# Kernel tuning notes

Measured on AMD Instinct MI355X. Metric: run time of the kernel, lower is better.

## Reference

```python
import jax, jax.numpy as jnp
import numpy as np

B, D, O = 16384, 1024, 1024
NUM_TASKS = 2
E = 4  # experts per group (2 task groups + 1 shared group)


def setup_inputs() -> dict:
    key = jax.random.key(0)
    ks = jax.random.split(key, 7)
    x = jax.random.normal(ks[0], (B, D), dtype=jnp.float32)
    # Stacked expert params: groups g in {task0, task1, shared}, each with E experts.
    W = jax.random.normal(ks[1], (3, E, D, O), dtype=jnp.float32) * 0.02  # Linear weight (in,out layout)
    b = jax.random.normal(ks[2], (3, E, O), dtype=jnp.float32) * 0.02
    # Per-task gates over (E specific + E shared) = 8 experts.
    Wg = jax.random.normal(ks[3], (NUM_TASKS, D, 2 * E), dtype=jnp.float32) * 0.02
    bg = jax.random.normal(ks[4], (NUM_TASKS, 2 * E), dtype=jnp.float32) * 0.02
    # Shared gate over all 3*E = 12 experts (is_top=False).
    Wgs = jax.random.normal(ks[5], (D, 3 * E), dtype=jnp.float32) * 0.02
    bgs = jax.random.normal(ks[6], (3 * E,), dtype=jnp.float32) * 0.02
    return {"x": x, "W": W, "b": b, "Wg": Wg, "bg": bg, "Wgs": Wgs, "bgs": bgs}


def reference(x, W, b, Wg, bg, Wgs, bgs):
    # All 12 experts share the same input (single-input branch): one batched GEMM.
    # h: [3, B, E, O]  (dropout is identity in eval mode)
    h = jax.nn.relu(jnp.einsum('bd,gedo->gbeo', x, W) + b[:, None, :, :])
    # Per-task gates: [T, B, 2E]
    sel_t = jax.nn.softmax(jnp.einsum('bd,tdm->tbm', x, Wg) + bg[:, None, :], axis=-1)
    outs = []
    for t in range(NUM_TASKS):
        mat = jnp.concatenate([h[t], h[2]], axis=1)  # [B, 2E, O]
        outs.append(jnp.einsum('bmo,bm->bo', mat, sel_t[t]))
    # Shared gate over all experts (is_top=False): [B, 3E]
    sel_s = jax.nn.softmax(x @ Wgs + bgs, axis=-1)
    mat_all = jnp.concatenate([h[0], h[1], h[2]], axis=1)  # [B, 3E, O]
    outs.append(jnp.einsum('bmo,bm->bo', mat_all, sel_s))
    return tuple(outs)
```

## Files before the change

kernel.cpp:

```cpp
#include <hip/hip_runtime.h>

typedef unsigned short ushort_t;
typedef __attribute__((ext_vector_type(8))) short short8;
typedef __attribute__((ext_vector_type(4))) float floatx4;

#define B_ROWS 16384
#define BO 16777216
#define MC 4096

__device__ __forceinline__ ushort_t f2bf(float f){
  unsigned u = __float_as_uint(f);
  u += 0x7fffu + ((u >> 16) & 1u);
  return (ushort_t)(u >> 16);
}
__device__ __forceinline__ float bf2f(ushort_t u){
  return __uint_as_float(((unsigned)u) << 16);
}

__device__ __forceinline__ void gld_lds16(void* l, const void* g){
  __builtin_amdgcn_global_load_lds(
      (__attribute__((address_space(1))) void*)(g),
      (__attribute__((address_space(3))) void*)(l), 16, 0, 0);
}

__global__ void cvt_x(const float* __restrict__ x, ushort_t* __restrict__ xb){
  const int i = (blockIdx.x * 256 + threadIdx.x) * 4;
  const floatx4 v = *(const floatx4*)(x + i);
  ushort4 o;
  o.x = f2bf(v[0]); o.y = f2bf(v[1]); o.z = f2bf(v[2]); o.w = f2bf(v[3]);
  *(ushort4*)(xb + i) = o;
}

__global__ void cvt_wt(const float* __restrict__ W, ushort_t* __restrict__ wt){
  __shared__ float t[64][65];
  const int blk = blockIdx.x;
  const int ge = blk >> 8, dt = (blk >> 4) & 15, ot = blk & 15;
  const float* src = W + ((size_t)ge << 20) + (size_t)(dt * 64) * 1024 + ot * 64;
  const int c4 = (threadIdx.x & 15) * 4, r0 = threadIdx.x >> 4;
#pragma unroll
  for (int p = 0; p < 4; ++p){
    const int r = r0 + p * 16;
    const floatx4 v = *(const floatx4*)(src + (size_t)r * 1024 + c4);
    t[r][c4] = v[0]; t[r][c4+1] = v[1]; t[r][c4+2] = v[2]; t[r][c4+3] = v[3];
  }
  __syncthreads();
  ushort_t* dst = wt + ((size_t)ge << 20) + (size_t)(ot * 64) * 1024 + dt * 64;
  const int d4 = (threadIdx.x & 15) * 4, o0 = threadIdx.x >> 4;
#pragma unroll
  for (int p = 0; p < 4; ++p){
    const int o = o0 + p * 16;
    ushort4 ov;
    ov.x = f2bf(t[d4][o]);   ov.y = f2bf(t[d4+1][o]);
    ov.z = f2bf(t[d4+2][o]); ov.w = f2bf(t[d4+3][o]);
    *(ushort4*)(dst + (size_t)o * 1024 + d4) = ov;
  }
}

__global__ void cvt_wg(const float* __restrict__ Wg, const float* __restrict__ bg,
                       const float* __restrict__ Wgs, const float* __restrict__ bgs,
                       ushort_t* __restrict__ wgcat, float* __restrict__ biascat){
  const int m = blockIdx.x;
#pragma unroll
  for (int j = 0; j < 4; ++j){
    const int d = j * 256 + threadIdx.x;
    float v;
    if (m < 16)      v = Wg[((size_t)((m >> 3) * 1024 + d)) * 8 + (m & 7)];
    else if (m < 28) v = Wgs[(size_t)d * 12 + (m - 16)];
    else             v = 0.f;
    wgcat[m * 1024 + d] = f2bf(v);
  }
  if (threadIdx.x == 0){
    float bv;
    if (m < 16)      bv = bg[m];
    else if (m < 28) bv = bgs[m - 16];
    else             bv = -1e30f;
    biascat[m] = bv;
  }
}

__global__ __launch_bounds__(256) void gates_mfma(
    const ushort_t* __restrict__ xb, const ushort_t* __restrict__ wgcat,
    const float* __restrict__ biascat, float* __restrict__ selT)
{
  __shared__ __align__(16) char gsm[20480];
  const int tid = threadIdx.x;
  const int lane = tid & 63;
  const int w = tid >> 6;
  const int lr = lane & 15;
  const int brow = blockIdx.x * 128;

  const int sc = (((tid & 7) ^ ((tid >> 3) & 7)) << 4);
  const char* aS = (const char*)xb + (size_t)(brow + (tid >> 3)) * 2048 + sc;
  const char* bS = (const char*)wgcat + (size_t)(tid >> 3) * 2048 + sc;

  const int kx0 = (((lane >> 4) << 4)) ^ ((lane & 7) << 4);
  const int kx1 = (64 + ((lane >> 4) << 4)) ^ ((lane & 7) << 4);

  int aOff[2], bOff[2];
#pragma unroll
  for (int m = 0; m < 2; ++m) aOff[m] = (w * 32 + m * 16 + lr) * 128;
#pragma unroll
  for (int n = 0; n < 2; ++n) bOff[n] = 16384 + (n * 16 + lr) * 128;

  const floatx4 fz = {0.f, 0.f, 0.f, 0.f};
  floatx4 hacc[2][2];
#pragma unroll
  for (int m = 0; m < 2; ++m)
#pragma unroll
    for (int n = 0; n < 2; ++n) hacc[m][n] = fz;

  for (int kt = 0; kt < 16; ++kt){
    const size_t ko = (size_t)kt * 128;
#pragma unroll
    for (int j = 0; j < 4; ++j)
      gld_lds16(gsm + j * 4096 + w * 1024, aS + (size_t)j * 65536 + ko);
    gld_lds16(gsm + 16384 + w * 1024, bS + ko);
    __syncthreads();
    short8 av[2][2], bv[2][2];
#pragma unroll
    for (int m = 0; m < 2; ++m){
      av[m][0] = *(const short8*)(gsm + aOff[m] + kx0);
      av[m][1] = *(const short8*)(gsm + aOff[m] + kx1);
    }
#pragma unroll
    for (int n = 0; n < 2; ++n){
      bv[n][0] = *(const short8*)(gsm + bOff[n] + kx0);
      bv[n][1] = *(const short8*)(gsm + bOff[n] + kx1);
    }
#pragma unroll
    for (int m = 0; m < 2; ++m)
#pragma unroll
      for (int n = 0; n < 2; ++n){
        hacc[m][n] = __builtin_amdgcn_mfma_f32_16x16x32_bf16(av[m][0], bv[n][0], hacc[m][n], 0, 0, 0);
        hacc[m][n] = __builtin_amdgcn_mfma_f32_16x16x32_bf16(av[m][1], bv[n][1], hacc[m][n], 0, 0, 0);
      }
    __syncthreads();
  }

  const float bc0 = biascat[lr];
  const float bc1 = biascat[16 + lr];
#pragma unroll
  for (int m = 0; m < 2; ++m){
#pragma unroll
    for (int r = 0; r < 4; ++r){
      float l0 = hacc[m][0][r] + bc0;
      float l1 = hacc[m][1][r] + bc1;
      float mx0 = l0;
#pragma unroll
      for (int s = 1; s < 8; s <<= 1) mx0 = fmaxf(mx0, __shfl_xor(mx0, s, 64));
      float e0 = __expf(l0 - mx0);
      float s0 = e0;
#pragma unroll
      for (int s = 1; s < 8; s <<= 1) s0 += __shfl_xor(s0, s, 64);
      float mx1 = l1;
#pragma unroll
      for (int s = 1; s < 16; s <<= 1) mx1 = fmaxf(mx1, __shfl_xor(mx1, s, 64));
      float e1 = __expf(l1 - mx1);
      float s1 = e1;
#pragma unroll
      for (int s = 1; s < 16; s <<= 1) s1 += __shfl_xor(s1, s, 64);
      const int row = brow + w * 32 + m * 16 + ((lane >> 4) << 2) + r;
      selT[(size_t)lr * B_ROWS + row] = e0 / s0;
      if (lr < 12) selT[(size_t)(16 + lr) * B_ROWS + row] = e1 / s1;
    }
  }
}

__global__ __launch_bounds__(512, 2) void pass1_gemm(
    const ushort_t* __restrict__ xb,
    const ushort_t* __restrict__ wt,
    const float* __restrict__ bias,
    ushort_t* __restrict__ h,
    int chunk_row0)
{
  __shared__ __align__(16) char smem[131072];
  const int tid  = threadIdx.x;
  const int lane = tid & 63;
  const int wv   = tid >> 6;
  const int wm   = wv >> 2;
  const int wn   = wv & 3;
  const int lr   = lane & 15;

  const int bid = blockIdx.x;
  const int L = (bid & 7) * 96 + (bid >> 3);
  const int mt = L / 48;
  const int rr = L % 48;
  const int ex = rr >> 2;
  const int nt = rr & 3;
  const int brow_l = mt * 256;
  const int browg  = chunk_row0 + brow_l;
  const int bcol   = nt * 256;

  const int sc = (((tid & 7) ^ ((tid >> 3) & 7)) << 4);
  const char* aSrc[2];
  const char* bSrc[2];
#pragma unroll
  for (int hh = 0; hh < 2; ++hh){
    aSrc[hh] = (const char*)xb + (size_t)(browg + hh * 128 + (tid >> 3)) * 2048 + sc;
    bSrc[hh] = (const char*)wt + ((size_t)ex << 21)
             + (size_t)(bcol + hh * 128 + (tid >> 3)) * 2048 + sc;
  }

  auto stageA = [&](int hh, int kt, int bo){
    char* d = smem + bo + hh * 16384 + wv * 1024;
    const char* s = aSrc[hh] + (size_t)kt * 128;
    gld_lds16(d, s);
    gld_lds16(d + 8192, s + 131072);
  };
  auto stageB = [&](int hh, int kt, int bo){
    char* d = smem + bo + 32768 + hh * 16384 + wv * 1024;
    const char* s = bSrc[hh] + (size_t)kt * 128;
    gld_lds16(d, s);
    gld_lds16(d + 8192, s + 131072);
  };

  const int kx0 = (((lane >> 4) << 4)) ^ ((lane & 7) << 4);
  const int kx1 = (64 + ((lane >> 4) << 4)) ^ ((lane & 7) << 4);
  int aOff[8], bOff[4];
#pragma unroll
  for (int m = 0; m < 8; ++m) aOff[m] = wm * 16384 + (m * 16 + lr) * 128;
#pragma unroll
  for (int n = 0; n < 4; ++n)
    bOff[n] = 32768 + (wn >> 1) * 16384 + ((wn & 1) * 64 + n * 16 + lr) * 128;

  const floatx4 fz = {0.f, 0.f, 0.f, 0.f};
  floatx4 hacc[8][4];
#pragma unroll
  for (int m = 0; m < 8; ++m)
#pragma unroll
    for (int n = 0; n < 4; ++n) hacc[m][n] = fz;

  stageA(0, 0, 0); stageA(1, 0, 0); stageB(0, 0, 0); stageB(1, 0, 0);
  stageB(0, 1, 65536); stageA(0, 1, 65536); stageA(1, 1, 65536);
  asm volatile("s_waitcnt vmcnt(6)" ::: "memory");
  __builtin_amdgcn_s_barrier();

#define LDF(X) (*(const short8*)(smem + (X)))
#define MFMA_(A, Bv, C) __builtin_amdgcn_mfma_f32_16x16x32_bf16(A, Bv, C, 0, 0, 0)
#define LGKM0_SB() { asm volatile("s_waitcnt lgkmcnt(0)" ::: "memory"); __builtin_amdgcn_sched_barrier(0); }

  for (int i = 0; i < 16; ++i){
    const int cur = (i & 1) << 16;
    const int nxt = cur ^ 65536;

    short8 a0[4][2], b0[2][2];
#pragma unroll
    for (int m = 0; m < 4; ++m){
      a0[m][0] = LDF(cur + aOff[m] + kx0);
      a0[m][1] = LDF(cur + aOff[m] + kx1);
    }
#pragma unroll
    for (int n = 0; n < 2; ++n){
      b0[n][0] = LDF(cur + bOff[n] + kx0);
      b0[n][1] = LDF(cur + bOff[n] + kx1);
    }
    if (i + 1 < 16) stageB(1, i + 1, nxt);
    __builtin_amdgcn_s_barrier();
    LGKM0_SB();
    __builtin_amdgcn_s_setprio(1);
#pragma unroll
    for (int m = 0; m < 4; ++m)
#pragma unroll
      for (int n = 0; n < 2; ++n){
        hacc[m][n] = MFMA_(a0[m][0], b0[n][0], hacc[m][n]);
        hacc[m][n] = MFMA_(a0[m][1], b0[n][1], hacc[m][n]);
      }
    __builtin_amdgcn_s_setprio(0);
    __builtin_amdgcn_s_barrier();

    short8 b1[2][2];
#pragma unroll
    for (int n = 0; n < 2; ++n){
      b1[n][0] = LDF(cur + bOff[2 + n] + kx0);
      b1[n][1] = LDF(cur + bOff[2 + n] + kx1);
    }
    __builtin_amdgcn_s_barrier();
    LGKM0_SB();
    __builtin_amdgcn_s_setprio(1);
#pragma unroll
    for (int m = 0; m < 4; ++m)
#pragma unroll
      for (int n = 0; n < 2; ++n){
        hacc[m][2 + n] = MFMA_(a0[m][0], b1[n][0], hacc[m][2 + n]);
        hacc[m][2 + n] = MFMA_(a0[m][1], b1[n][1], hacc[m][2 + n]);
      }
    __builtin_amdgcn_s_setprio(0);
    __builtin_amdgcn_s_barrier();

    short8 a1[4][2];
#pragma unroll
    for (int m = 0; m < 4; ++m){
      a1[m][0] = LDF(cur + aOff[4 + m] + kx0);
      a1[m][1] = LDF(cur + aOff[4 + m] + kx1);
    }
    if (i + 2 < 16) stageB(0, i + 2, cur);
    __builtin_amdgcn_s_barrier();
    LGKM0_SB();
    __builtin_amdgcn_s_setprio(1);
#pragma unroll
    for (int m = 0; m < 4; ++m)
#pragma unroll
      for (int n = 0; n < 2; ++n){
        hacc[4 + m][n] = MFMA_(a1[m][0], b0[n][0], hacc[4 + m][n]);
        hacc[4 + m][n] = MFMA_(a1[m][1], b0[n][1], hacc[4 + m][n]);
      }
    __builtin_amdgcn_s_setprio(0);
    __builtin_amdgcn_s_barrier();

    if (i + 2 < 16) { stageA(0, i + 2, cur); stageA(1, i + 2, cur); }
    __builtin_amdgcn_s_barrier();
    __builtin_amdgcn_s_setprio(1);
#pragma unroll
    for (int m = 0; m < 4; ++m)
#pragma unroll
      for (int n = 0; n < 2; ++n){
        hacc[4 + m][2 + n] = MFMA_(a1[m][0], b1[n][0], hacc[4 + m][2 + n]);
        hacc[4 + m][2 + n] = MFMA_(a1[m][1], b1[n][1], hacc[4 + m][2 + n]);
      }
    __builtin_amdgcn_s_setprio(0);
    if (i < 14)       { asm volatile("s_waitcnt vmcnt(6)" ::: "memory"); }
    else if (i == 14) { asm volatile("s_waitcnt vmcnt(0)" ::: "memory"); }
    __builtin_amdgcn_s_barrier();
  }

  const int colb = bcol + wn * 64 + lr;
  float bi[4];
#pragma unroll
  for (int n = 0; n < 4; ++n) bi[n] = bias[ex * 1024 + colb + n * 16];
  ushort_t* hbase = h + ((size_t)ex * MC) * 1024;
#pragma unroll
  for (int m = 0; m < 8; ++m){
#pragma unroll
    for (int r = 0; r < 4; ++r){
      const int row = brow_l + wm * 128 + m * 16 + ((lane >> 4) << 2) + r;
      ushort_t* hp = hbase + (size_t)row * 1024 + colb;
#pragma unroll
      for (int n = 0; n < 4; ++n){
        float v = hacc[m][n][r] + bi[n];
        hp[n * 16] = f2bf(fmaxf(v, 0.f));
      }
    }
  }
#undef LDF
#undef MFMA_
#undef LGKM0_SB
}

__global__ __launch_bounds__(256) void combine_kernel(
    const ushort_t* __restrict__ h,
    const float* __restrict__ selT,
    float* __restrict__ out,
    int row0)
{
  const int tid = threadIdx.x;
  const int lb  = blockIdx.x * 2 + (tid >> 7);
  const int b   = row0 + lb;
  const int c   = (tid & 127) * 8;
  const ushort_t* hp = h + (size_t)lb * 1024 + c;

  float a0[8], a1[8], as_[8];
#pragma unroll
  for (int k = 0; k < 8; ++k){ a0[k] = 0.f; a1[k] = 0.f; as_[k] = 0.f; }

#pragma unroll
  for (int e = 0; e < 4; ++e){
    const float w0 = selT[(size_t)e * B_ROWS + b];
    const float ws = selT[(size_t)(16 + e) * B_ROWS + b];
    const short8 hv = *(const short8*)(hp + (size_t)e * (MC * 1024));
#pragma unroll
    for (int k = 0; k < 8; ++k){
      const float f = bf2f((ushort_t)hv[k]);
      a0[k] += w0 * f; as_[k] += ws * f;
    }
  }
#pragma unroll
  for (int e = 0; e < 4; ++e){
    const float w1 = selT[(size_t)(8 + e) * B_ROWS + b];
    const float ws = selT[(size_t)(20 + e) * B_ROWS + b];
    const short8 hv = *(const short8*)(hp + (size_t)(4 + e) * (MC * 1024));
#pragma unroll
    for (int k = 0; k < 8; ++k){
      const float f = bf2f((ushort_t)hv[k]);
      a1[k] += w1 * f; as_[k] += ws * f;
    }
  }
#pragma unroll
  for (int e = 0; e < 4; ++e){
    const float w0 = selT[(size_t)(4 + e) * B_ROWS + b];
    const float w1 = selT[(size_t)(12 + e) * B_ROWS + b];
    const float ws = selT[(size_t)(24 + e) * B_ROWS + b];
    const short8 hv = *(const short8*)(hp + (size_t)(8 + e) * (MC * 1024));
#pragma unroll
    for (int k = 0; k < 8; ++k){
      const float f = bf2f((ushort_t)hv[k]);
      a0[k] += w0 * f; a1[k] += w1 * f; as_[k] += ws * f;
    }
  }

  float* o0 = out + (size_t)b * 1024 + c;
  *(floatx4*)(o0)     = *(const floatx4*)(a0);
  *(floatx4*)(o0 + 4) = *(const floatx4*)(a0 + 4);
  float* o1 = o0 + BO;
  *(floatx4*)(o1)     = *(const floatx4*)(a1);
  *(floatx4*)(o1 + 4) = *(const floatx4*)(a1 + 4);
  float* o2 = o1 + BO;
  *(floatx4*)(o2)     = *(const floatx4*)(as_);
  *(floatx4*)(o2 + 4) = *(const floatx4*)(as_ + 4);
}

__global__ void gates_kernel(const float* __restrict__ x,
                             const float* __restrict__ Wg,
                             const float* __restrict__ bg,
                             const float* __restrict__ Wgs,
                             const float* __restrict__ bgs,
                             float* __restrict__ selT)
{
  const int lane = threadIdx.x & 63;
  const int w    = threadIdx.x >> 6;
  const int b    = blockIdx.x * 4 + w;
  const float* xr = x + (size_t)b * 1024;
  float acc[28];
#pragma unroll
  for (int m = 0; m < 28; ++m) acc[m] = 0.f;
#pragma unroll
  for (int j = 0; j < 4; ++j){
    const int d0 = (j * 64 + lane) * 4;
    const floatx4 xv = *(const floatx4*)(xr + d0);
#pragma unroll
    for (int q = 0; q < 4; ++q){
      const float xs = xv[q];
      const int d = d0 + q;
      const float* g0 = Wg + d * 8;
      const float* g1 = Wg + 8192 + d * 8;
      const float* gs = Wgs + d * 12;
#pragma unroll
      for (int m = 0; m < 8; ++m)  acc[m]      += xs * g0[m];
#pragma unroll
      for (int m = 0; m < 8; ++m)  acc[8 + m]  += xs * g1[m];
#pragma unroll
      for (int m = 0; m < 12; ++m) acc[16 + m] += xs * gs[m];
    }
  }
#pragma unroll
  for (int m = 0; m < 28; ++m){
    float v = acc[m];
#pragma unroll
    for (int off = 1; off < 64; off <<= 1) v += __shfl_xor(v, off, 64);
    acc[m] = v;
  }
  if (lane == 0){
    float e0[8], e1[8], es[12];
    float mx0 = -1e30f, mx1 = -1e30f, mxs = -1e30f;
#pragma unroll
    for (int m = 0; m < 8; ++m){  e0[m] = acc[m]      + bg[m];     mx0 = fmaxf(mx0, e0[m]); }
#pragma unroll
    for (int m = 0; m < 8; ++m){  e1[m] = acc[8 + m]  + bg[8 + m]; mx1 = fmaxf(mx1, e1[m]); }
#pragma unroll
    for (int m = 0; m < 12; ++m){ es[m] = acc[16 + m] + bgs[m];    mxs = fmaxf(mxs, es[m]); }
    float s0 = 0.f, s1 = 0.f, ss = 0.f;
#pragma unroll
    for (int m = 0; m < 8; ++m){  e0[m] = __expf(e0[m] - mx0); s0 += e0[m]; }
#pragma unroll
    for (int m = 0; m < 8; ++m){  e1[m] = __expf(e1[m] - mx1); s1 += e1[m]; }
#pragma unroll
    for (int m = 0; m < 12; ++m){ es[m] = __expf(es[m] - mxs); ss += es[m]; }
    const float r0 = 1.f / s0, r1 = 1.f / s1, rs = 1.f / ss;
#pragma unroll
    for (int m = 0; m < 8; ++m)  selT[(size_t)m * B_ROWS + b]        = e0[m] * r0;
#pragma unroll
    for (int m = 0; m < 8; ++m)  selT[(size_t)(8 + m) * B_ROWS + b]  = e1[m] * r1;
#pragma unroll
    for (int m = 0; m < 12; ++m) selT[(size_t)(16 + m) * B_ROWS + b] = es[m] * rs;
  }
}

__global__ __launch_bounds__(256, 2) void moe_kernel(
    const ushort_t* __restrict__ xb,
    const ushort_t* __restrict__ wt,
    const float* __restrict__ bias,
    const float* __restrict__ selT,
    float* __restrict__ out)
{
  __shared__ __align__(16) char smem[24576];
  const int tid  = threadIdx.x;
  const int lane = tid & 63;
  const int wid  = tid >> 6;
  const int wm   = wid >> 1;
  const int wn   = wid & 1;
  const int brow = (blockIdx.x >> 4) << 7;
  const int bcol = (blockIdx.x & 15) << 6;
  const int rstg = tid >> 3;
  const int scol = ((tid & 7) << 4) ^ ((rstg & 7) << 4);
  size_t aoff[4], boff[2];
#pragma unroll
  for (int i = 0; i < 4; ++i) aoff[i] = (size_t)(brow + i * 32 + rstg) * 2048 + scol;
#pragma unroll
  for (int i = 0; i < 2; ++i) boff[i] = (size_t)(bcol + i * 32 + rstg) * 2048 + scol;
  char* aldst = smem + wid * 1024;
  char* bldst = smem + 16384 + wid * 1024;
  const int kl   = (lane >> 4) << 4;
  const int swzr = (lane & 7) << 4;
  int arow[4], brw[2];
#pragma unroll
  for (int m = 0; m < 4; ++m) arow[m] = (wm * 64 + m * 16 + (lane & 15)) * 128;
#pragma unroll
  for (int n = 0; n < 2; ++n) brw[n] = 16384 + (wn * 32 + n * 16 + (lane & 15)) * 128;
  const floatx4 fz = {0.f, 0.f, 0.f, 0.f};
  floatx4 o0a[4][2], o1a[4][2], osa[4][2];
#pragma unroll
  for (int m = 0; m < 4; ++m)
#pragma unroll
    for (int n = 0; n < 2; ++n){ o0a[m][n] = fz; o1a[m][n] = fz; osa[m][n] = fz; }
  const int c0 = bcol + wn * 32 + (lane & 15);
  const int rb = brow + wm * 64 + ((lane >> 4) << 2);
  for (int ex = 0; ex < 12; ++ex){
    floatx4 hacc[4][2];
#pragma unroll
    for (int m = 0; m < 4; ++m)
#pragma unroll
      for (int n = 0; n < 2; ++n) hacc[m][n] = fz;
    const size_t wbase = (size_t)ex << 21;
    for (int kt = 0; kt < 16; ++kt){
      const size_t ko = (size_t)kt << 7;
#pragma unroll
      for (int i = 0; i < 4; ++i)
        gld_lds16(aldst + i * 4096, (const char*)xb + aoff[i] + ko);
#pragma unroll
      for (int i = 0; i < 2; ++i)
        gld_lds16(bldst + i * 4096, (const char*)wt + wbase + boff[i] + ko);
      __syncthreads();
#pragma unroll
      for (int kk = 0; kk < 2; ++kk){
        short8 av[4], bv[2];
        const int kb = (kk << 6) + kl;
#pragma unroll
        for (int m = 0; m < 4; ++m)
          av[m] = *(const short8*)(smem + arow[m] + (kb ^ swzr));
#pragma unroll
        for (int n = 0; n < 2; ++n)
          bv[n] = *(const short8*)(smem + brw[n] + (kb ^ swzr));
#pragma unroll
        for (int m = 0; m < 4; ++m)
#pragma unroll
          for (int n = 0; n < 2; ++n)
            hacc[m][n] = __builtin_amdgcn_mfma_f32_16x16x32_bf16(av[m], bv[n], hacc[m][n], 0, 0, 0);
      }
      __syncthreads();
    }
    const int g = ex >> 2, e = ex & 3;
    const float bi0 = bias[ex * 1024 + c0];
    const float bi1 = bias[ex * 1024 + c0 + 16];
    int i0, i1, is_;
    if (g == 0)      { i0 = e;     i1 = -1;     is_ = 16 + e; }
    else if (g == 1) { i0 = -1;    i1 = 8 + e;  is_ = 20 + e; }
    else             { i0 = 4 + e; i1 = 12 + e; is_ = 24 + e; }
#pragma unroll
    for (int m = 0; m < 4; ++m){
      const int rg = rb + m * 16;
      const floatx4 wsv = *(const floatx4*)(selT + (size_t)is_ * B_ROWS + rg);
      floatx4 w0 = fz, w1 = fz;
      if (i0 >= 0) w0 = *(const floatx4*)(selT + (size_t)i0 * B_ROWS + rg);
      if (i1 >= 0) w1 = *(const floatx4*)(selT + (size_t)i1 * B_ROWS + rg);
#pragma unroll
      for (int n = 0; n < 2; ++n){
        const float bi = n ? bi1 : bi0;
#pragma unroll
        for (int r = 0; r < 4; ++r){
          float hv = hacc[m][n][r] + bi;
          hv = fmaxf(hv, 0.f);
          osa[m][n][r] += wsv[r] * hv;
          o0a[m][n][r] += w0[r] * hv;
          o1a[m][n][r] += w1[r] * hv;
        }
      }
    }
  }
#pragma unroll
  for (int m = 0; m < 4; ++m){
#pragma unroll
    for (int n = 0; n < 2; ++n){
#pragma unroll
      for (int r = 0; r < 4; ++r){
        const size_t idx = (size_t)(rb + m * 16 + r) * 1024 + (c0 + (n << 4));
        out[idx]          = o0a[m][n][r];
        out[idx + BO]     = o1a[m][n][r];
        out[idx + 2 * BO] = osa[m][n][r];
      }
    }
  }
}

extern "C" void kernel_launch(void* const* d_in, const int* in_sizes, int n_in,
                              void* d_out, int out_size, void* d_ws, size_t ws_size,
                              hipStream_t stream) {
  const float* x   = (const float*)d_in[0];
  const float* W   = (const float*)d_in[1];
  const float* b   = (const float*)d_in[2];
  const float* Wg  = (const float*)d_in[3];
  const float* bg  = (const float*)d_in[4];
  const float* Wgs = (const float*)d_in[5];
  const float* bgs = (const float*)d_in[6];
  float* out = (float*)d_out;

  char* ws = (char*)d_ws;
  ushort_t* xb   = (ushort_t*)ws;
  ushort_t* wtp  = (ushort_t*)(ws + 33554432);
  float*    selT = (float*)(ws + 58720256);
  ushort_t* wgc  = (ushort_t*)(ws + 60555264);
  float*    bcat = (float*)(ws + 60620800);
  ushort_t* hbuf = (ushort_t*)(ws + 67108864);

  const bool two_pass = ws_size >= (size_t)(67108864 + 12 * MC * 1024 * 2);

  cvt_x<<<dim3(16384), dim3(256), 0, stream>>>(x, xb);
  cvt_wt<<<dim3(3072), dim3(256), 0, stream>>>(W, wtp);

  if (two_pass){
    cvt_wg<<<dim3(32), dim3(256), 0, stream>>>(Wg, bg, Wgs, bgs, wgc, bcat);
    gates_mfma<<<dim3(128), dim3(256), 0, stream>>>(xb, wgc, bcat, selT);
    for (int c = 0; c < 16384 / MC; ++c){
      pass1_gemm<<<dim3((MC / 256) * 48), dim3(512), 0, stream>>>(xb, wtp, b, hbuf, c * MC);
      combine_kernel<<<dim3(MC / 2), dim3(256), 0, stream>>>(hbuf, selT, out, c * MC);
    }
  } else {
    gates_kernel<<<dim3(4096), dim3(256), 0, stream>>>(x, Wg, bg, Wgs, bgs, selT);
    moe_kernel<<<dim3(2048), dim3(256), 0, stream>>>(xb, wtp, b, selT, out);
  }
}
```

Before: 606.8 us.

## Make each GEMM block loop over three experts with a persistent grid of 256

The GEMM grid drops from 768 blocks to 256. Each block now runs a 48-step K loop that covers three consecutive experts for the same 256x256 output tile, writing the bias+ReLU epilogue and resetting accumulators after every 16 steps. The aim is to keep the pipeline primed across experts, removing per-block prologue and drain and the partial last wave (768 blocks at 2 per CU over 256 CUs). The trade-off is fewer, longer blocks, epilogue stores that stall the pipeline mid-loop, and reduced reuse of the A tile in cache, since x is reloaded for each expert.

```diff
diff --git a/kernel.cpp b/kernel.cpp
--- a/kernel.cpp
+++ b/kernel.cpp
@@ -180,36 +180,37 @@
   const int wm   = wv >> 2;
   const int wn   = wv & 3;
   const int lr   = lane & 15;
+  const int NT   = 48;
 
   const int bid = blockIdx.x;
-  const int L = (bid & 7) * 96 + (bid >> 3);
-  const int mt = L / 48;
-  const int rr = L % 48;
-  const int ex = rr >> 2;
-  const int nt = rr & 3;
+  const int L = (bid & 7) * 32 + (bid >> 3);
+  const int eg = L >> 6;
+  const int nt = (L >> 4) & 3;
+  const int mt = L & 15;
   const int brow_l = mt * 256;
   const int browg  = chunk_row0 + brow_l;
   const int bcol   = nt * 256;
 
   const int sc = (((tid & 7) ^ ((tid >> 3) & 7)) << 4);
   const char* aSrc[2];
-  const char* bSrc[2];
+  size_t bOffBase[2];
 #pragma unroll
   for (int hh = 0; hh < 2; ++hh){
     aSrc[hh] = (const char*)xb + (size_t)(browg + hh * 128 + (tid >> 3)) * 2048 + sc;
-    bSrc[hh] = (const char*)wt + ((size_t)ex << 21)
-             + (size_t)(bcol + hh * 128 + (tid >> 3)) * 2048 + sc;
+    bOffBase[hh] = (size_t)(bcol + hh * 128 + (tid >> 3)) * 2048 + sc;
   }
 
   auto stageA = [&](int hh, int kt, int bo){
     char* d = smem + bo + hh * 16384 + wv * 1024;
-    const char* s = aSrc[hh] + (size_t)kt * 128;
+    const char* s = aSrc[hh] + (size_t)(kt & 15) * 128;
     gld_lds16(d, s);
     gld_lds16(d + 8192, s + 131072);
   };
   auto stageB = [&](int hh, int kt, int bo){
+    const int exk = eg * 3 + (kt >> 4);
     char* d = smem + bo + 32768 + hh * 16384 + wv * 1024;
-    const char* s = bSrc[hh] + (size_t)kt * 128;
+    const char* s = (const char*)wt + ((size_t)exk << 21) + bOffBase[hh]
+                  + (size_t)(kt & 15) * 128;
     gld_lds16(d, s);
     gld_lds16(d + 8192, s + 131072);
   };
@@ -229,6 +230,32 @@
   for (int m = 0; m < 8; ++m)
 #pragma unroll
     for (int n = 0; n < 4; ++n) hacc[m][n] = fz;
+
+  const int colb = bcol + wn * 64 + lr;
+  float bi[3][4];
+#pragma unroll
+  for (int ee = 0; ee < 3; ++ee)
+#pragma unroll
+    for (int n = 0; n < 4; ++n)
+      bi[ee][n] = bias[(eg * 3 + ee) * 1024 + colb + n * 16];
+
+  auto EPI = [&](int el){
+    ushort_t* hbase = h + ((size_t)(eg * 3 + el) * MC) * 1024;
+#pragma unroll
+    for (int m = 0; m < 8; ++m){
+#pragma unroll
+      for (int r = 0; r < 4; ++r){
+        const int row = brow_l + wm * 128 + m * 16 + ((lane >> 4) << 2) + r;
+        ushort_t* hp = hbase + (size_t)row * 1024 + colb;
+#pragma unroll
+        for (int n = 0; n < 4; ++n){
+          float v = hacc[m][n][r] + bi[el][n];
+          hp[n * 16] = f2bf(fmaxf(v, 0.f));
+          hacc[m][n][r] = 0.f;
+        }
+      }
+    }
+  };
 
   stageA(0, 0, 0); stageA(1, 0, 0); stageB(0, 0, 0); stageB(1, 0, 0);
   stageB(0, 1, 65536); stageA(0, 1, 65536); stageA(1, 1, 65536);
@@ -239,7 +266,7 @@
 #define MFMA_(A, Bv, C) __builtin_amdgcn_mfma_f32_16x16x32_bf16(A, Bv, C, 0, 0, 0)
 #define LGKM0_SB() { asm volatile("s_waitcnt lgkmcnt(0)" ::: "memory"); __builtin_amdgcn_sched_barrier(0); }
 
-  for (int i = 0; i < 16; ++i){
+  for (int i = 0; i < NT; ++i){
     const int cur = (i & 1) << 16;
     const int nxt = cur ^ 65536;
 
@@ -254,7 +281,7 @@
       b0[n][0] = LDF(cur + bOff[n] + kx0);
       b0[n][1] = LDF(cur + bOff[n] + kx1);
     }
-    if (i + 1 < 16) stageB(1, i + 1, nxt);
+    if (i + 1 < NT) stageB(1, i + 1, nxt);
     __builtin_amdgcn_s_barrier();
     LGKM0_SB();
     __builtin_amdgcn_s_setprio(1);
@@ -293,7 +320,7 @@
       a1[m][0] = LDF(cur + aOff[4 + m] + kx0);
       a1[m][1] = LDF(cur + aOff[4 + m] + kx1);
     }
-    if (i + 2 < 16) stageB(0, i + 2, cur);
+    if (i + 2 < NT) stageB(0, i + 2, cur);
     __builtin_amdgcn_s_barrier();
     LGKM0_SB();
     __builtin_amdgcn_s_setprio(1);
@@ -307,7 +334,7 @@
     __builtin_amdgcn_s_setprio(0);
     __builtin_amdgcn_s_barrier();
 
-    if (i + 2 < 16) { stageA(0, i + 2, cur); stageA(1, i + 2, cur); }
+    if (i + 2 < NT) { stageA(0, i + 2, cur); stageA(1, i + 2, cur); }
     __builtin_amdgcn_s_barrier();
     __builtin_amdgcn_s_setprio(1);
 #pragma unroll
@@ -318,28 +345,10 @@
         hacc[4 + m][2 + n] = MFMA_(a1[m][1], b1[n][1], hacc[4 + m][2 + n]);
       }
     __builtin_amdgcn_s_setprio(0);
-    if (i < 14)       { asm volatile("s_waitcnt vmcnt(6)" ::: "memory"); }
-    else if (i == 14) { asm volatile("s_waitcnt vmcnt(0)" ::: "memory"); }
-    __builtin_amdgcn_s_barrier();
-  }
-
-  const int colb = bcol + wn * 64 + lr;
-  float bi[4];
-#pragma unroll
-  for (int n = 0; n < 4; ++n) bi[n] = bias[ex * 1024 + colb + n * 16];
-  ushort_t* hbase = h + ((size_t)ex * MC) * 1024;
-#pragma unroll
-  for (int m = 0; m < 8; ++m){
-#pragma unroll
-    for (int r = 0; r < 4; ++r){
-      const int row = brow_l + wm * 128 + m * 16 + ((lane >> 4) << 2) + r;
-      ushort_t* hp = hbase + (size_t)row * 1024 + colb;
-#pragma unroll
-      for (int n = 0; n < 4; ++n){
-        float v = hacc[m][n][r] + bi[n];
-        hp[n * 16] = f2bf(fmaxf(v, 0.f));
-      }
-    }
+    if ((i & 15) == 15) EPI(i >> 4);
+    if (i < NT - 2)       { asm volatile("s_waitcnt vmcnt(6)" ::: "memory"); }
+    else if (i == NT - 2) { asm volatile("s_waitcnt vmcnt(0)" ::: "memory"); }
+    __builtin_amdgcn_s_barrier();
   }
 #undef LDF
 #undef MFMA_
@@ -619,7 +628,7 @@
     cvt_wg<<<dim3(32), dim3(256), 0, stream>>>(Wg, bg, Wgs, bgs, wgc, bcat);
     gates_mfma<<<dim3(128), dim3(256), 0, stream>>>(xb, wgc, bcat, selT);
     for (int c = 0; c < 16384 / MC; ++c){
-      pass1_gemm<<<dim3((MC / 256) * 48), dim3(512), 0, stream>>>(xb, wtp, b, hbuf, c * MC);
+      pass1_gemm<<<dim3(256), dim3(512), 0, stream>>>(xb, wtp, b, hbuf, c * MC);
       combine_kernel<<<dim3(MC / 2), dim3(256), 0, stream>>>(hbuf, selT, out, c * MC);
     }
   } else {
```

Measured after the change: 671.2 us. +10.6%, slower.

## Restructure GEMM main loop into two phases and transpose MFMA for packed stores

Applied to the files above, without the earlier changes.

The pass1 GEMM inner loop goes from four MFMA phases with barriers to two. All B fragments are loaded up front, and the A tile for the next k-step is prefetched early together with one B half, which changes the staging order and the vmcnt waits. MFMA operands are swapped so each lane holds four consecutive output columns. The epilogue can then load bias as float4 and write packed 8-byte bf16 stores instead of scalar 2-byte stores. This cuts barrier count and store instructions, at the cost of more live fragment registers and a tighter LDS buffer reuse schedule.

```diff
diff --git a/kernel.cpp b/kernel.cpp
--- a/kernel.cpp
+++ b/kernel.cpp
@@ -180,6 +180,7 @@
   const int wm   = wv >> 2;
   const int wn   = wv & 3;
   const int lr   = lane & 15;
+  const int NT   = 16;
 
   const int bid = blockIdx.x;
   const int L = (bid & 7) * 96 + (bid >> 3);
@@ -201,11 +202,14 @@
              + (size_t)(bcol + hh * 128 + (tid >> 3)) * 2048 + sc;
   }
 
-  auto stageA = [&](int hh, int kt, int bo){
-    char* d = smem + bo + hh * 16384 + wv * 1024;
-    const char* s = aSrc[hh] + (size_t)kt * 128;
-    gld_lds16(d, s);
-    gld_lds16(d + 8192, s + 131072);
+  auto stageA = [&](int kt, int bo){
+#pragma unroll
+    for (int hh = 0; hh < 2; ++hh){
+      char* d = smem + bo + hh * 16384 + wv * 1024;
+      const char* s = aSrc[hh] + (size_t)kt * 128;
+      gld_lds16(d, s);
+      gld_lds16(d + 8192, s + 131072);
+    }
   };
   auto stageB = [&](int hh, int kt, int bo){
     char* d = smem + bo + 32768 + hh * 16384 + wv * 1024;
@@ -230,20 +234,21 @@
 #pragma unroll
     for (int n = 0; n < 4; ++n) hacc[m][n] = fz;
 
-  stageA(0, 0, 0); stageA(1, 0, 0); stageB(0, 0, 0); stageB(1, 0, 0);
-  stageB(0, 1, 65536); stageA(0, 1, 65536); stageA(1, 1, 65536);
-  asm volatile("s_waitcnt vmcnt(6)" ::: "memory");
+  stageA(0, 0);
+  stageB(0, 0, 0); stageB(1, 0, 0);
+  stageB(0, 1, 65536);
+  asm volatile("s_waitcnt vmcnt(2)" ::: "memory");
   __builtin_amdgcn_s_barrier();
 
 #define LDF(X) (*(const short8*)(smem + (X)))
 #define MFMA_(A, Bv, C) __builtin_amdgcn_mfma_f32_16x16x32_bf16(A, Bv, C, 0, 0, 0)
 #define LGKM0_SB() { asm volatile("s_waitcnt lgkmcnt(0)" ::: "memory"); __builtin_amdgcn_sched_barrier(0); }
 
-  for (int i = 0; i < 16; ++i){
+  for (int i = 0; i < NT; ++i){
     const int cur = (i & 1) << 16;
     const int nxt = cur ^ 65536;
 
-    short8 a0[4][2], b0[2][2];
+    short8 a0[4][2], b0[2][2], b1[2][2];
 #pragma unroll
     for (int m = 0; m < 4; ++m){
       a0[m][0] = LDF(cur + aOff[m] + kx0);
@@ -253,8 +258,10 @@
     for (int n = 0; n < 2; ++n){
       b0[n][0] = LDF(cur + bOff[n] + kx0);
       b0[n][1] = LDF(cur + bOff[n] + kx1);
-    }
-    if (i + 1 < 16) stageB(1, i + 1, nxt);
+      b1[n][0] = LDF(cur + bOff[2 + n] + kx0);
+      b1[n][1] = LDF(cur + bOff[2 + n] + kx1);
+    }
+    if (i + 1 < NT){ stageA(i + 1, nxt); stageB(1, i + 1, nxt); }
     __builtin_amdgcn_s_barrier();
     LGKM0_SB();
     __builtin_amdgcn_s_setprio(1);
@@ -262,18 +269,21 @@
     for (int m = 0; m < 4; ++m)
 #pragma unroll
       for (int n = 0; n < 2; ++n){
-        hacc[m][n] = MFMA_(a0[m][0], b0[n][0], hacc[m][n]);
-        hacc[m][n] = MFMA_(a0[m][1], b0[n][1], hacc[m][n]);
+        hacc[m][n]     = MFMA_(b0[n][0], a0[m][0], hacc[m][n]);
+        hacc[m][n]     = MFMA_(b0[n][1], a0[m][1], hacc[m][n]);
+        hacc[m][2 + n] = MFMA_(b1[n][0], a0[m][0], hacc[m][2 + n]);
+        hacc[m][2 + n] = MFMA_(b1[n][1], a0[m][1], hacc[m][2 + n]);
       }
     __builtin_amdgcn_s_setprio(0);
     __builtin_amdgcn_s_barrier();
 
-    short8 b1[2][2];
-#pragma unroll
-    for (int n = 0; n < 2; ++n){
-      b1[n][0] = LDF(cur + bOff[2 + n] + kx0);
-      b1[n][1] = LDF(cur + bOff[2 + n] + kx1);
-    }
+    short8 a1[4][2];
+#pragma unroll
+    for (int m = 0; m < 4; ++m){
+      a1[m][0] = LDF(cur + aOff[4 + m] + kx0);
+      a1[m][1] = LDF(cur + aOff[4 + m] + kx1);
+    }
+    if (i + 2 < NT) stageB(0, i + 2, cur);
     __builtin_amdgcn_s_barrier();
     LGKM0_SB();
     __builtin_amdgcn_s_setprio(1);
@@ -281,64 +291,38 @@
     for (int m = 0; m < 4; ++m)
 #pragma unroll
       for (int n = 0; n < 2; ++n){
-        hacc[m][2 + n] = MFMA_(a0[m][0], b1[n][0], hacc[m][2 + n]);
-        hacc[m][2 + n] = MFMA_(a0[m][1], b1[n][1], hacc[m][2 + n]);
+        hacc[4 + m][n]     = MFMA_(b0[n][0], a1[m][0], hacc[4 + m][n]);
+        hacc[4 + m][n]     = MFMA_(b0[n][1], a1[m][1], hacc[4 + m][n]);
+        hacc[4 + m][2 + n] = MFMA_(b1[n][0], a1[m][0], hacc[4 + m][2 + n]);
+        hacc[4 + m][2 + n] = MFMA_(b1[n][1], a1[m][1], hacc[4 + m][2 + n]);
       }
     __builtin_amdgcn_s_setprio(0);
+    if (i < NT - 2)       { asm volatile("s_waitcnt vmcnt(2)" ::: "memory"); }
+    else if (i == NT - 2) { asm volatile("s_waitcnt vmcnt(0)" ::: "memory"); }
     __builtin_amdgcn_s_barrier();
-
-    short8 a1[4][2];
-#pragma unroll
-    for (int m = 0; m < 4; ++m){
-      a1[m][0] = LDF(cur + aOff[4 + m] + kx0);
-      a1[m][1] = LDF(cur + aOff[4 + m] + kx1);
-    }
-    if (i + 2 < 16) stageB(0, i + 2, cur);
-    __builtin_amdgcn_s_barrier();
-    LGKM0_SB();
-    __builtin_amdgcn_s_setprio(1);
-#pragma unroll
-    for (int m = 0; m < 4; ++m)
-#pragma unroll
-      for (int n = 0; n < 2; ++n){
-        hacc[4 + m][n] = MFMA_(a1[m][0], b0[n][0], hacc[4 + m][n]);
-        hacc[4 + m][n] = MFMA_(a1[m][1], b0[n][1], hacc[4 + m][n]);
-      }
-    __builtin_amdgcn_s_setprio(0);
-    __builtin_amdgcn_s_barrier();
-
-    if (i + 2 < 16) { stageA(0, i + 2, cur); stageA(1, i + 2, cur); }
-    __builtin_amdgcn_s_barrier();
-    __builtin_amdgcn_s_setprio(1);
-#pragma unroll
-    for (int m = 0; m < 4; ++m)
-#pragma unroll
-      for (int n = 0; n < 2; ++n){
-        hacc[4 + m][2 + n] = MFMA_(a1[m][0], b1[n][0], hacc[4 + m][2 + n]);
-        hacc[4 + m][2 + n] = MFMA_(a1[m][1], b1[n][1], hacc[4 + m][2 + n]);
-      }
-    __builtin_amdgcn_s_setprio(0);
-    if (i < 14)       { asm volatile("s_waitcnt vmcnt(6)" ::: "memory"); }
-    else if (i == 14) { asm volatile("s_waitcnt vmcnt(0)" ::: "memory"); }
-    __builtin_amdgcn_s_barrier();
-  }
-
-  const int colb = bcol + wn * 64 + lr;
-  float bi[4];
-#pragma unroll
-  for (int n = 0; n < 4; ++n) bi[n] = bias[ex * 1024 + colb + n * 16];
+  }
+
+  const int colb2 = bcol + wn * 64;
+  const int g4 = (lane >> 4) << 2;
+  floatx4 bv[4];
+#pragma unroll
+  for (int n = 0; n < 4; ++n)
+    bv[n] = *(const floatx4*)(bias + ex * 1024 + colb2 + n * 16 + g4);
   ushort_t* hbase = h + ((size_t)ex * MC) * 1024;
 #pragma unroll
   for (int m = 0; m < 8; ++m){
-#pragma unroll
-    for (int r = 0; r < 4; ++r){
-      const int row = brow_l + wm * 128 + m * 16 + ((lane >> 4) << 2) + r;
-      ushort_t* hp = hbase + (size_t)row * 1024 + colb;
-#pragma unroll
-      for (int n = 0; n < 4; ++n){
-        float v = hacc[m][n][r] + bi[n];
-        hp[n * 16] = f2bf(fmaxf(v, 0.f));
-      }
+    const int row = brow_l + wm * 128 + m * 16 + lr;
+    ushort_t* hp = hbase + (size_t)row * 1024 + colb2 + g4;
+#pragma unroll
+    for (int n = 0; n < 4; ++n){
+      const float v0 = fmaxf(hacc[m][n][0] + bv[n][0], 0.f);
+      const float v1 = fmaxf(hacc[m][n][1] + bv[n][1], 0.f);
+      const float v2 = fmaxf(hacc[m][n][2] + bv[n][2], 0.f);
+      const float v3 = fmaxf(hacc[m][n][3] + bv[n][3], 0.f);
+      uint2 pk;
+      pk.x = (unsigned)f2bf(v0) | ((unsigned)f2bf(v1) << 16);
+      pk.y = (unsigned)f2bf(v2) | ((unsigned)f2bf(v3) << 16);
+      *(uint2*)(hp + n * 16) = pk;
     }
   }
 #undef LDF
@@ -619,7 +603,7 @@
     cvt_wg<<<dim3(32), dim3(256), 0, stream>>>(Wg, bg, Wgs, bgs, wgc, bcat);
     gates_mfma<<<dim3(128), dim3(256), 0, stream>>>(xb, wgc, bcat, selT);
     for (int c = 0; c < 16384 / MC; ++c){
-      pass1_gemm<<<dim3((MC / 256) * 48), dim3(512), 0, stream>>>(xb, wtp, b, hbuf, c * MC);
+      pass1_gemm<<<dim3(768), dim3(512), 0, stream>>>(xb, wtp, b, hbuf, c * MC);
       combine_kernel<<<dim3(MC / 2), dim3(256), 0, stream>>>(hbuf, selT, out, c * MC);
     }
   } else {
```

Result: slower. 651.4 us (+7.4%).
